# Optimization experiments

Hardware: AMD Instinct MI355X
Metric: run time of the kernel (lower is better)

## Reference

```python
import jax, jax.numpy as jnp
import numpy as np

N_NODES = 100000
N_EDGES = 1600000
D_IN = 128
D_OUT = 5


def setup_inputs() -> dict:
    key = jax.random.key(0)
    k1, k2, k3, k4, k5 = jax.random.split(key, 5)
    x = jax.random.normal(k1, (N_NODES, D_IN), dtype=jnp.float32)
    edge_index = jax.random.randint(k2, (2, N_EDGES), 0, N_NODES, dtype=jnp.int64)
    scale = 1.0 / np.sqrt(D_IN)
    W_l = jax.random.normal(k3, (D_OUT, D_IN), dtype=jnp.float32) * scale
    b_l = jax.random.normal(k4, (D_OUT,), dtype=jnp.float32) * scale
    W_r = jax.random.normal(k5, (D_OUT, D_IN), dtype=jnp.float32) * scale
    return {"x": x, "edge_index": edge_index, "W_l": W_l, "b_l": b_l, "W_r": W_r}


def reference(x, edge_index, W_l, b_l, W_r):
    # PyG SAGEConv with aggr='mean', root_weight=True:
    # out_i = mean_{j: (j->i) in E} x_j @ W_l^T + b_l + x_i @ W_r^T
    n = x.shape[0]
    src = edge_index[0]
    dst = edge_index[1]
    msgs = x[src]  # [E, D_in] gather (irregular access)
    agg_sum = jax.ops.segment_sum(msgs, dst, num_segments=n)  # [N, D_in]
    deg = jax.ops.segment_sum(jnp.ones(src.shape, dtype=x.dtype), dst, num_segments=n)
    agg_mean = agg_sum / jnp.maximum(deg, 1.0)[:, None]  # zero-degree nodes -> 0
    out = agg_mean @ W_l.T + b_l + x @ W_r.T  # [N, D_out]
    return out
```

## Files before the change

kernel.cpp:

```cpp
#include <hip/hip_runtime.h>
#include <hip/hip_bf16.h>


#define N_NODES 100000
#define N_EDGES 1600000
#define D_IN 128
#define D_OUT 5

#define HL_STRIDE 8

#define BSHIFT 8
#define B_NODES 256
#define N_BUCKETS 392
#define CAP 5120

#define SC_EPT 8
#define SC_EPB (256 * SC_EPT)
#define SC_GRID ((N_EDGES + SC_EPB - 1) / SC_EPB)

#define PROJ_BLOCKS ((N_NODES * 16 + 255) / 256)
#define FUSED_GRID (PROJ_BLOCKS + SC_GRID)

#define FXS 262144.0f
#define FXB 16777216u
#define FXBF 16777216.0f
#define INV_FXS (1.0f / 262144.0f)

typedef unsigned long long u64;
typedef unsigned int u32;

__global__ __launch_bounds__(256) void proj_scatter_kernel(
    const float* __restrict__ x,
    const float* __restrict__ Wl,
    const float* __restrict__ Wr,
    float* __restrict__ hl,
    float* __restrict__ hr,
    const int* __restrict__ ei,
    unsigned int* __restrict__ sorted,
    int* __restrict__ cursor)
{
    if (blockIdx.x < PROJ_BLOCKS) {
        int node = (blockIdx.x * 256 + threadIdx.x) >> 4;
        int k    = threadIdx.x & 15;
        if (node >= N_NODES) return;

        const float4* xr = (const float4*)(x + (size_t)node * D_IN + k * 8);
        float4 x0 = xr[0];
        float4 x1 = xr[1];

        float s[10];
#pragma unroll
        for (int o = 0; o < 10; ++o) {
            const float* w = (o < 5 ? Wl + o * D_IN : Wr + (o - 5) * D_IN) + k * 8;
            float4 w0 = ((const float4*)w)[0];
            float4 w1 = ((const float4*)w)[1];
            s[o] = x0.x * w0.x + x0.y * w0.y + x0.z * w0.z + x0.w * w0.w
                 + x1.x * w1.x + x1.y * w1.y + x1.z * w1.z + x1.w * w1.w;
        }

#pragma unroll
        for (int o = 0; o < 10; ++o) {
            s[o] += __shfl_xor(s[o], 8, 64);
            s[o] += __shfl_xor(s[o], 4, 64);
            s[o] += __shfl_xor(s[o], 2, 64);
            s[o] += __shfl_xor(s[o], 1, 64);
        }

        if (k == 0) {
            float* pl = hl + (size_t)node * HL_STRIDE;
            pl[0] = s[0]; pl[1] = s[1]; pl[2] = s[2]; pl[3] = s[3]; pl[4] = s[4];
            float* pr = hr + (size_t)node * 5;
            pr[0] = s[5]; pr[1] = s[6]; pr[2] = s[7]; pr[3] = s[8]; pr[4] = s[9];
        }
    } else {
        __shared__ int hist[N_BUCKETS];
        __shared__ int basepos[N_BUCKETS];

        const int tid = threadIdx.x;
        for (int i = tid; i < N_BUCKETS; i += 256) hist[i] = 0;
        __syncthreads();

        const int blk = blockIdx.x - PROJ_BLOCKS;
        const int e0  = blk * SC_EPB + tid * SC_EPT;

        int srcv[SC_EPT], dstv[SC_EPT], slot[SC_EPT];
        bool valid[SC_EPT];

        if (e0 + SC_EPT <= N_EDGES) {
            const int4* s4 = (const int4*)(ei + e0);
            const int4* d4 = (const int4*)(ei + N_EDGES + e0);
            int4 sa = s4[0], sb = s4[1], da = d4[0], db = d4[1];
            srcv[0]=sa.x; srcv[1]=sa.y; srcv[2]=sa.z; srcv[3]=sa.w;
            srcv[4]=sb.x; srcv[5]=sb.y; srcv[6]=sb.z; srcv[7]=sb.w;
            dstv[0]=da.x; dstv[1]=da.y; dstv[2]=da.z; dstv[3]=da.w;
            dstv[4]=db.x; dstv[5]=db.y; dstv[6]=db.z; dstv[7]=db.w;
#pragma unroll
            for (int q = 0; q < SC_EPT; ++q) valid[q] = true;
        } else {
#pragma unroll
            for (int q = 0; q < SC_EPT; ++q) {
                int e = e0 + q;
                valid[q] = (e < N_EDGES);
                srcv[q] = valid[q] ? ei[e] : 0;
                dstv[q] = valid[q] ? ei[N_EDGES + e] : 0;
            }
        }

#pragma unroll
        for (int q = 0; q < SC_EPT; ++q) {
            if (valid[q]) {
                int b = dstv[q] >> BSHIFT;
                slot[q] = atomicAdd(&hist[b], 1);
            }
        }
        __syncthreads();

        for (int b = tid; b < N_BUCKETS; b += 256) {
            int c = hist[b];
            if (c > 0) basepos[b] = atomicAdd(&cursor[b], c);
        }
        __syncthreads();

#pragma unroll
        for (int q = 0; q < SC_EPT; ++q) {
            if (valid[q]) {
                int b = dstv[q] >> BSHIFT;
                int r = dstv[q] & (B_NODES - 1);
                unsigned int rec = ((unsigned int)r << 17) | (unsigned int)srcv[q];
                sorted[(size_t)b * CAP + basepos[b] + slot[q]] = rec;
            }
        }
    }
}

__global__ __launch_bounds__(1024) void agg_kernel(
    const unsigned int* __restrict__ sorted,
    const int* __restrict__ cursor,
    const float* __restrict__ hl,
    const float* __restrict__ hr,
    const float* __restrict__ bias,
    float* __restrict__ out)
{
    __shared__ u64 acc[B_NODES * 3];

    const int b   = blockIdx.x;
    const int tid = threadIdx.x;

    for (int i = tid; i < B_NODES * 3; i += 1024) acc[i] = 0ull;
    __syncthreads();

    const int cnt = cursor[b];
    const unsigned int* sp = sorted + (size_t)b * CAP;
    const int nvec = cnt >> 2;

    for (int it = tid; it < nvec; it += 1024) {
        uint4 v = ((const uint4*)sp)[it];
        unsigned int rr[4] = { v.x, v.y, v.z, v.w };
#pragma unroll
        for (int q = 0; q < 4; ++q) {
            int src = (int)(rr[q] & 0x1FFFFu);
            int r   = (int)(rr[q] >> 17);
            const float* p = hl + (size_t)src * HL_STRIDE;
            float4 h = *(const float4*)p;
            float  e = p[4];
            u32 f0 = __float2uint_rn(fmaf(h.x, FXS, FXBF));
            u32 f1 = __float2uint_rn(fmaf(h.y, FXS, FXBF));
            u32 f2 = __float2uint_rn(fmaf(h.z, FXS, FXBF));
            u32 f3 = __float2uint_rn(fmaf(h.w, FXS, FXBF));
            u32 f4 = __float2uint_rn(fmaf(e,   FXS, FXBF));
            u64* a = acc + r * 3;
            atomicAdd(&a[0], ((u64)f1 << 32) | f0);
            atomicAdd(&a[1], ((u64)f3 << 32) | f2);
            atomicAdd(&a[2], ((u64)f4 << 32) | 1u);
        }
    }
    for (int i = (nvec << 2) + tid; i < cnt; i += 1024) {
        unsigned int v = sp[i];
        int src = (int)(v & 0x1FFFFu);
        int r   = (int)(v >> 17);
        const float* p = hl + (size_t)src * HL_STRIDE;
        float4 h = *(const float4*)p;
        float  e = p[4];
        u32 f0 = __float2uint_rn(fmaf(h.x, FXS, FXBF));
        u32 f1 = __float2uint_rn(fmaf(h.y, FXS, FXBF));
        u32 f2 = __float2uint_rn(fmaf(h.z, FXS, FXBF));
        u32 f3 = __float2uint_rn(fmaf(h.w, FXS, FXBF));
        u32 f4 = __float2uint_rn(fmaf(e,   FXS, FXBF));
        u64* a = acc + r * 3;
        atomicAdd(&a[0], ((u64)f1 << 32) | f0);
        atomicAdd(&a[1], ((u64)f3 << 32) | f2);
        atomicAdd(&a[2], ((u64)f4 << 32) | 1u);
    }
    __syncthreads();

    const int nodebase = b << BSHIFT;
    for (int n = tid; n < B_NODES; n += 1024) {
        int node = nodebase + n;
        if (node >= N_NODES) continue;
        u64 w0 = acc[n * 3 + 0];
        u64 w1 = acc[n * 3 + 1];
        u64 w2 = acc[n * 3 + 2];
        u32 deg = (u32)(w2 & 0xFFFFFFFFu);
        u32 db  = deg * FXB;
        int i0 = (int)((u32)(w0 & 0xFFFFFFFFu) - db);
        int i1 = (int)((u32)(w0 >> 32)         - db);
        int i2 = (int)((u32)(w1 & 0xFFFFFFFFu) - db);
        int i3 = (int)((u32)(w1 >> 32)         - db);
        int i4 = (int)((u32)(w2 >> 32)         - db);

        float rec = INV_FXS / fmaxf((float)deg, 1.0f);
        const float* h = hr + (size_t)node * 5;
        float* o = out + (size_t)node * 5;
        o[0] = (float)i0 * rec + bias[0] + h[0];
        o[1] = (float)i1 * rec + bias[1] + h[1];
        o[2] = (float)i2 * rec + bias[2] + h[2];
        o[3] = (float)i3 * rec + bias[3] + h[3];
        o[4] = (float)i4 * rec + bias[4] + h[4];
    }
}

extern "C" void kernel_launch(void* const* d_in, const int* in_sizes, int n_in,
                              void* d_out, int out_size, void* d_ws, size_t ws_size,
                              hipStream_t stream) {
    const float* x    = (const float*)d_in[0];
    const int*   ei   = (const int*)d_in[1];
    const float* Wl   = (const float*)d_in[2];
    const float* bl   = (const float*)d_in[3];
    const float* Wr   = (const float*)d_in[4];
    float*       out  = (float*)d_out;

    float*        hl     = (float*)d_ws;
    float*        hr     = hl + (size_t)N_NODES * HL_STRIDE;
    unsigned int* sorted = (unsigned int*)(hr + (size_t)N_NODES * 5);
    int*          cursor = (int*)(sorted + (size_t)N_BUCKETS * CAP);

    hipMemsetAsync(cursor, 0, N_BUCKETS * sizeof(int), stream);

    proj_scatter_kernel<<<FUSED_GRID, 256, 0, stream>>>(
        x, Wl, Wr, hl, hr, ei, sorted, cursor);

    agg_kernel<<<N_BUCKETS, 1024, 0, stream>>>(sorted, cursor, hl, hr, bl, out);
}
```

Baseline: 141.7 us.

## Rebalance buckets to 256, interleave proj/scatter blocks, cache weights in LDS

Changes the dst bucketing from 392 buckets of 256 nodes to 256 buckets of 391 nodes, so the aggregation grid matches the CU count and per-bucket capacity grows. Projection blocks now handle 64 nodes each, with W_l/W_r staged in shared memory, and are interleaved 2:1 with scatter blocks via blockIdx%3 so both phases run concurrently. hr gets stride 8 with vectorized float4 stores, and the aggregation loop issues all four gathers before the atomics to expose memory-level parallelism. The cost is an integer division by 391 per edge, and larger buckets raise LDS atomic contention per block.

```diff
diff --git a/kernel.cpp b/kernel.cpp
--- a/kernel.cpp
+++ b/kernel.cpp
@@ -9,17 +9,17 @@
 
 #define HL_STRIDE 8
 
-#define BSHIFT 8
-#define B_NODES 256
-#define N_BUCKETS 392
-#define CAP 5120
+#define B_NODES 391
+#define N_BUCKETS 256
+#define CAP 7168
 
 #define SC_EPT 8
 #define SC_EPB (256 * SC_EPT)
-#define SC_GRID ((N_EDGES + SC_EPB - 1) / SC_EPB)
-
-#define PROJ_BLOCKS ((N_NODES * 16 + 255) / 256)
-#define FUSED_GRID (PROJ_BLOCKS + SC_GRID)
+#define SC_GRID 782
+
+#define PROJ_NPB 64
+#define PROJ_BLOCKS 1564
+#define FUSED_GRID 2346
 
 #define FXS 262144.0f
 #define FXB 16777216u
@@ -39,48 +39,69 @@
     unsigned int* __restrict__ sorted,
     int* __restrict__ cursor)
 {
-    if (blockIdx.x < PROJ_BLOCKS) {
-        int node = (blockIdx.x * 256 + threadIdx.x) >> 4;
-        int k    = threadIdx.x & 15;
-        if (node >= N_NODES) return;
-
-        const float4* xr = (const float4*)(x + (size_t)node * D_IN + k * 8);
-        float4 x0 = xr[0];
-        float4 x1 = xr[1];
-
-        float s[10];
-#pragma unroll
-        for (int o = 0; o < 10; ++o) {
-            const float* w = (o < 5 ? Wl + o * D_IN : Wr + (o - 5) * D_IN) + k * 8;
-            float4 w0 = ((const float4*)w)[0];
-            float4 w1 = ((const float4*)w)[1];
-            s[o] = x0.x * w0.x + x0.y * w0.y + x0.z * w0.z + x0.w * w0.w
-                 + x1.x * w1.x + x1.y * w1.y + x1.z * w1.z + x1.w * w1.w;
-        }
-
-#pragma unroll
-        for (int o = 0; o < 10; ++o) {
-            s[o] += __shfl_xor(s[o], 8, 64);
-            s[o] += __shfl_xor(s[o], 4, 64);
-            s[o] += __shfl_xor(s[o], 2, 64);
-            s[o] += __shfl_xor(s[o], 1, 64);
-        }
-
-        if (k == 0) {
-            float* pl = hl + (size_t)node * HL_STRIDE;
-            pl[0] = s[0]; pl[1] = s[1]; pl[2] = s[2]; pl[3] = s[3]; pl[4] = s[4];
-            float* pr = hr + (size_t)node * 5;
-            pr[0] = s[5]; pr[1] = s[6]; pr[2] = s[7]; pr[3] = s[8]; pr[4] = s[9];
+    __shared__ __align__(16) float smem[1280];
+    const int tid = threadIdx.x;
+    const int role = blockIdx.x % 3;
+
+    if (role != 2) {
+        const int pblk = (blockIdx.x / 3) * 2 + role;
+
+        for (int i = tid; i < 320; i += 256) {
+            float4 v = (i < 160) ? ((const float4*)Wl)[i]
+                                 : ((const float4*)Wr)[i - 160];
+            ((float4*)smem)[i] = v;
+        }
+        __syncthreads();
+
+        const int g = tid >> 4;
+        const int k = tid & 15;
+        const float* wk = smem + k * 8;
+        const int node0 = pblk * PROJ_NPB + g * 4;
+
+#pragma unroll
+        for (int it = 0; it < 4; ++it) {
+            const int node = node0 + it;
+            if (node < N_NODES) {
+                const float4* xr = (const float4*)(x + (size_t)node * D_IN + k * 8);
+                float4 x0 = xr[0];
+                float4 x1 = xr[1];
+
+                float s[10];
+#pragma unroll
+                for (int o = 0; o < 10; ++o) {
+                    const float4* w4 = (const float4*)(wk + o * 128);
+                    float4 w0 = w4[0];
+                    float4 w1 = w4[1];
+                    s[o] = x0.x * w0.x + x0.y * w0.y + x0.z * w0.z + x0.w * w0.w
+                         + x1.x * w1.x + x1.y * w1.y + x1.z * w1.z + x1.w * w1.w;
+                }
+
+#pragma unroll
+                for (int o = 0; o < 10; ++o) {
+                    s[o] += __shfl_xor(s[o], 8, 64);
+                    s[o] += __shfl_xor(s[o], 4, 64);
+                    s[o] += __shfl_xor(s[o], 2, 64);
+                    s[o] += __shfl_xor(s[o], 1, 64);
+                }
+
+                if (k == 0) {
+                    float* pl = hl + (size_t)node * HL_STRIDE;
+                    *(float4*)pl = make_float4(s[0], s[1], s[2], s[3]);
+                    pl[4] = s[4];
+                    float* pr = hr + (size_t)node * HL_STRIDE;
+                    *(float4*)pr = make_float4(s[5], s[6], s[7], s[8]);
+                    pr[4] = s[9];
+                }
+            }
         }
     } else {
-        __shared__ int hist[N_BUCKETS];
-        __shared__ int basepos[N_BUCKETS];
-
-        const int tid = threadIdx.x;
-        for (int i = tid; i < N_BUCKETS; i += 256) hist[i] = 0;
-        __syncthreads();
-
-        const int blk = blockIdx.x - PROJ_BLOCKS;
+        int* hist    = (int*)smem;
+        int* basepos = hist + N_BUCKETS;
+
+        if (tid < N_BUCKETS) hist[tid] = 0;
+        __syncthreads();
+
+        const int blk = blockIdx.x / 3;
         const int e0  = blk * SC_EPB + tid * SC_EPT;
 
         int srcv[SC_EPT], dstv[SC_EPT], slot[SC_EPT];
@@ -109,24 +130,24 @@
 #pragma unroll
         for (int q = 0; q < SC_EPT; ++q) {
             if (valid[q]) {
-                int b = dstv[q] >> BSHIFT;
+                unsigned b = (unsigned)dstv[q] / 391u;
                 slot[q] = atomicAdd(&hist[b], 1);
             }
         }
         __syncthreads();
 
-        for (int b = tid; b < N_BUCKETS; b += 256) {
-            int c = hist[b];
-            if (c > 0) basepos[b] = atomicAdd(&cursor[b], c);
+        if (tid < N_BUCKETS) {
+            int c = hist[tid];
+            if (c > 0) basepos[tid] = atomicAdd(&cursor[tid], c);
         }
         __syncthreads();
 
 #pragma unroll
         for (int q = 0; q < SC_EPT; ++q) {
             if (valid[q]) {
-                int b = dstv[q] >> BSHIFT;
-                int r = dstv[q] & (B_NODES - 1);
-                unsigned int rec = ((unsigned int)r << 17) | (unsigned int)srcv[q];
+                unsigned b = (unsigned)dstv[q] / 391u;
+                unsigned r = (unsigned)dstv[q] - b * 391u;
+                unsigned rec = (r << 17) | (unsigned)srcv[q];
                 sorted[(size_t)b * CAP + basepos[b] + slot[q]] = rec;
             }
         }
@@ -155,24 +176,33 @@
 
     for (int it = tid; it < nvec; it += 1024) {
         uint4 v = ((const uint4*)sp)[it];
-        unsigned int rr[4] = { v.x, v.y, v.z, v.w };
-#pragma unroll
-        for (int q = 0; q < 4; ++q) {
-            int src = (int)(rr[q] & 0x1FFFFu);
-            int r   = (int)(rr[q] >> 17);
-            const float* p = hl + (size_t)src * HL_STRIDE;
-            float4 h = *(const float4*)p;
-            float  e = p[4];
-            u32 f0 = __float2uint_rn(fmaf(h.x, FXS, FXBF));
-            u32 f1 = __float2uint_rn(fmaf(h.y, FXS, FXBF));
-            u32 f2 = __float2uint_rn(fmaf(h.z, FXS, FXBF));
-            u32 f3 = __float2uint_rn(fmaf(h.w, FXS, FXBF));
-            u32 f4 = __float2uint_rn(fmaf(e,   FXS, FXBF));
-            u64* a = acc + r * 3;
-            atomicAdd(&a[0], ((u64)f1 << 32) | f0);
-            atomicAdd(&a[1], ((u64)f3 << 32) | f2);
-            atomicAdd(&a[2], ((u64)f4 << 32) | 1u);
-        }
+        int s0 = (int)(v.x & 0x1FFFFu), r0 = (int)(v.x >> 17);
+        int s1 = (int)(v.y & 0x1FFFFu), r1 = (int)(v.y >> 17);
+        int s2 = (int)(v.z & 0x1FFFFu), r2 = (int)(v.z >> 17);
+        int s3 = (int)(v.w & 0x1FFFFu), r3 = (int)(v.w >> 17);
+
+        const float* p0 = hl + (size_t)s0 * HL_STRIDE;
+        const float* p1 = hl + (size_t)s1 * HL_STRIDE;
+        const float* p2 = hl + (size_t)s2 * HL_STRIDE;
+        const float* p3 = hl + (size_t)s3 * HL_STRIDE;
+        float4 h0 = *(const float4*)p0; float e0 = p0[4];
+        float4 h1 = *(const float4*)p1; float e1 = p1[4];
+        float4 h2 = *(const float4*)p2; float e2 = p2[4];
+        float4 h3 = *(const float4*)p3; float e3 = p3[4];
+
+#define EMIT(hh, ee, rr)                                                     \
+        {                                                                    \
+            u32 f0 = __float2uint_rn(fmaf((hh).x, FXS, FXBF));               \
+            u32 f1 = __float2uint_rn(fmaf((hh).y, FXS, FXBF));               \
+            u32 f2 = __float2uint_rn(fmaf((hh).z, FXS, FXBF));               \
+            u32 f3 = __float2uint_rn(fmaf((hh).w, FXS, FXBF));               \
+            u32 f4 = __float2uint_rn(fmaf((ee),   FXS, FXBF));               \
+            u64* a = acc + (rr) * 3;                                         \
+            atomicAdd(&a[0], ((u64)f1 << 32) | f0);                          \
+            atomicAdd(&a[1], ((u64)f3 << 32) | f2);                          \
+            atomicAdd(&a[2], ((u64)f4 << 32) | 1u);                          \
+        }
+        EMIT(h0, e0, r0) EMIT(h1, e1, r1) EMIT(h2, e2, r2) EMIT(h3, e3, r3)
     }
     for (int i = (nvec << 2) + tid; i < cnt; i += 1024) {
         unsigned int v = sp[i];
@@ -181,19 +211,12 @@
         const float* p = hl + (size_t)src * HL_STRIDE;
         float4 h = *(const float4*)p;
         float  e = p[4];
-        u32 f0 = __float2uint_rn(fmaf(h.x, FXS, FXBF));
-        u32 f1 = __float2uint_rn(fmaf(h.y, FXS, FXBF));
-        u32 f2 = __float2uint_rn(fmaf(h.z, FXS, FXBF));
-        u32 f3 = __float2uint_rn(fmaf(h.w, FXS, FXBF));
-        u32 f4 = __float2uint_rn(fmaf(e,   FXS, FXBF));
-        u64* a = acc + r * 3;
-        atomicAdd(&a[0], ((u64)f1 << 32) | f0);
-        atomicAdd(&a[1], ((u64)f3 << 32) | f2);
-        atomicAdd(&a[2], ((u64)f4 << 32) | 1u);
-    }
+        EMIT(h, e, r)
+    }
+#undef EMIT
     __syncthreads();
 
-    const int nodebase = b << BSHIFT;
+    const int nodebase = b * B_NODES;
     for (int n = tid; n < B_NODES; n += 1024) {
         int node = nodebase + n;
         if (node >= N_NODES) continue;
@@ -209,7 +232,7 @@
         int i4 = (int)((u32)(w2 >> 32)         - db);
 
         float rec = INV_FXS / fmaxf((float)deg, 1.0f);
-        const float* h = hr + (size_t)node * 5;
+        const float* h = hr + (size_t)node * HL_STRIDE;
         float* o = out + (size_t)node * 5;
         o[0] = (float)i0 * rec + bias[0] + h[0];
         o[1] = (float)i1 * rec + bias[1] + h[1];
@@ -231,7 +254,7 @@
 
     float*        hl     = (float*)d_ws;
     float*        hr     = hl + (size_t)N_NODES * HL_STRIDE;
-    unsigned int* sorted = (unsigned int*)(hr + (size_t)N_NODES * 5);
+    unsigned int* sorted = (unsigned int*)(hr + (size_t)N_NODES * HL_STRIDE);
     int*          cursor = (int*)(sorted + (size_t)N_BUCKETS * CAP);
 
     hipMemsetAsync(cursor, 0, N_BUCKETS * sizeof(int), stream);
```

Measured after the change: 145.8 us. 2.9% more time.
